# Kernel tuning notes

Hardware: AMD Instinct MI355X
Metric: run time of the kernel (lower is better)

The kernel has to match this reference:

```python
import jax, jax.numpy as jnp
import numpy as np

B, S, E = 2, 2048, 1024
H = 16
D = E // H  # 64
SCALE = D ** -0.5


def setup_inputs() -> dict:
    key = jax.random.key(0)
    ks = jax.random.split(key, 9)
    w = lambda k: jax.random.normal(k, (E, E), dtype=jnp.float32) * 0.02
    b = lambda k: jax.random.normal(k, (E,), dtype=jnp.float32) * 0.02
    return {
        "hidden_states": jax.random.normal(ks[0], (B, S, E), dtype=jnp.float32),
        "q_w": w(ks[1]), "q_b": b(ks[2]),
        "k_w": w(ks[3]), "k_b": b(ks[4]),
        "v_w": w(ks[5]), "v_b": b(ks[6]),
        "o_w": w(ks[7]), "o_b": b(ks[8]),
    }


def reference(hidden_states, q_w, q_b, k_w, k_b, v_w, v_b, o_w, o_b):
    dtype = hidden_states.dtype
    # torch Linear: y = x @ W^T + b
    q = hidden_states @ q_w.T + q_b
    k = hidden_states @ k_w.T + k_b
    v = hidden_states @ v_w.T + v_b
    # [B,S,E] -> [B*H, S, D]
    split = lambda t: t.reshape(B, S, H, D).transpose(0, 2, 1, 3).reshape(B * H, S, D)
    q, k, v = split(q), split(k), split(v)
    # upcast_attention: fp32 QK^T, scaled (baddbmm with beta=0, no mask)
    scores = SCALE * jnp.einsum("bqd,bkd->bqk", q.astype(jnp.float32), k.astype(jnp.float32))
    # upcast_softmax: fp32 softmax over last dim (transpose_qk=False), cast back
    probs = jax.nn.softmax(scores, axis=-1).astype(dtype)
    # PV bmm, merge heads, out_proj (dropout p=0.0 -> identity)
    out = jnp.einsum("bqk,bkd->bqd", probs, v)
    out = out.reshape(B, H, S, D).transpose(0, 2, 1, 3).reshape(B, S, E)
    return out @ o_w.T + o_b
```

## Files before the change

kernel.cpp:

```cpp
#include <hip/hip_runtime.h>

typedef __bf16 bf16x8 __attribute__((ext_vector_type(8)));
typedef __bf16 bf16x4 __attribute__((ext_vector_type(4)));
typedef float  f32x4  __attribute__((ext_vector_type(4)));
typedef float  f32x16 __attribute__((ext_vector_type(16)));
typedef unsigned int u32x4 __attribute__((ext_vector_type(4)));

#define CS 0.18033688011112042f

__device__ __forceinline__ float fast_exp2(float x) {
    return __builtin_amdgcn_exp2f(x);
}

__device__ __forceinline__ void gload_lds16(const __bf16* g, __bf16* l) {
    __builtin_amdgcn_global_load_lds(
        (const __attribute__((address_space(1))) void*)g,
        (__attribute__((address_space(3))) void*)l, 16, 0, 0);
}

__device__ __forceinline__ f32x4 MFMA(bf16x8 a, bf16x8 b, f32x4 c) {
    return __builtin_amdgcn_mfma_f32_16x16x32_bf16(a, b, c, 0, 0, 0);
}
__device__ __forceinline__ f32x16 MFMA32(bf16x8 a, bf16x8 b, f32x16 c) {
    return __builtin_amdgcn_mfma_f32_32x32x16_bf16(a, b, c, 0, 0, 0);
}

__device__ __forceinline__ unsigned pk2(float a, float b) {
    union { __bf16 h[2]; unsigned u; } x;
    x.h[0] = (__bf16)a; x.h[1] = (__bf16)b;
    return x.u;
}

__device__ __forceinline__ void swap32(unsigned &a, unsigned &b) {
    asm volatile("v_permlane32_swap_b32 %0, %1" : "+v"(a), "+v"(b));
}

__global__ __launch_bounds__(256) void cvt5_kernel(
    const float* __restrict__ s0, const float* __restrict__ s1,
    const float* __restrict__ s2, const float* __restrict__ s3,
    const float* __restrict__ s4,
    __bf16* __restrict__ d0, __bf16* __restrict__ d1, __bf16* __restrict__ d2,
    __bf16* __restrict__ d3, __bf16* __restrict__ d4)
{
    int blk = blockIdx.x;
    const float* src; __bf16* dst; int base;
    if (blk < 4096)      { src = s0; dst = d0; base = blk; }
    else if (blk < 5120) { src = s1; dst = d1; base = blk - 4096; }
    else if (blk < 6144) { src = s2; dst = d2; base = blk - 5120; }
    else if (blk < 7168) { src = s3; dst = d3; base = blk - 6144; }
    else                 { src = s4; dst = d4; base = blk - 7168; }
    int i = base * 1024 + threadIdx.x * 4;
    float4 v = *(const float4*)(src + i);
    bf16x4 o;
    o[0] = (__bf16)v.x; o[1] = (__bf16)v.y; o[2] = (__bf16)v.z; o[3] = (__bf16)v.w;
    *(bf16x4*)(dst + i) = o;
}

template <typename OutT, int BN>
__device__ __forceinline__ void gemm_core(const __bf16* __restrict__ A,
                                          const __bf16* __restrict__ W,
                                          const float* __restrict__ bias,
                                          OutT* __restrict__ C,
                                          int m0, int n0, bool vtrans, float oscale)
{
    constexpr int NJ  = BN / 32;
    constexpr int BCH = BN / 32;
    __shared__ __bf16 As[128 * 64];
    __shared__ __bf16 Bs[BN * 64];

    const int tid  = threadIdx.x;
    const int lane = tid & 63;
    const int w    = tid >> 6;
    const int wm   = w & 1;
    const int wn   = w >> 1;
    const int s    = lane & 15;
    const int q    = lane >> 4;

    const int srow = lane >> 3;
    const int scol = (lane & 7) ^ srow;

    f32x4 acc[4][NJ];
#pragma unroll
    for (int i = 0; i < 4; i++)
#pragma unroll
        for (int j = 0; j < NJ; j++)
#pragma unroll
            for (int r = 0; r < 4; r++) acc[i][j][r] = 0.0f;

    for (int k0 = 0; k0 < 1024; k0 += 64) {
        __syncthreads();
#pragma unroll
        for (int t = 0; t < 4; t++) {
            int chunk = w * 4 + t;
            int row   = chunk * 8 + srow;
            gload_lds16(A + (size_t)(m0 + row) * 1024 + k0 + scol * 8,
                        &As[chunk * 512]);
        }
#pragma unroll
        for (int t = 0; t < BCH; t++) {
            int chunk = w * BCH + t;
            int row   = chunk * 8 + srow;
            gload_lds16(W + (size_t)(n0 + row) * 1024 + k0 + scol * 8,
                        &Bs[chunk * 512]);
        }
        __syncthreads();

#pragma unroll
        for (int kk = 0; kk < 2; kk++) {
            bf16x8 af[4], bf[NJ];
#pragma unroll
            for (int i = 0; i < 4; i++) {
                int row = wm * 64 + i * 16 + s;
                af[i] = *(const bf16x8*)&As[row * 64 + ((((kk << 2) + q) ^ (row & 7)) << 3)];
            }
#pragma unroll
            for (int j = 0; j < NJ; j++) {
                int row = wn * (BN / 2) + j * 16 + s;
                bf[j] = *(const bf16x8*)&Bs[row * 64 + ((((kk << 2) + q) ^ (row & 7)) << 3)];
            }
#pragma unroll
            for (int i = 0; i < 4; i++)
#pragma unroll
                for (int j = 0; j < NJ; j++)
                    acc[i][j] = MFMA(af[i], bf[j], acc[i][j]);
        }
    }

    if (vtrans) {
        __bf16* Vt = (__bf16*)C;
#pragma unroll
        for (int j = 0; j < NJ; j++) {
            int col = n0 + wn * (BN / 2) + j * 16 + s;
            int h   = col >> 6;
            int d   = col & 63;
            float bv = bias[col];
#pragma unroll
            for (int i = 0; i < 4; i++) {
                int rowb = m0 + wm * 64 + i * 16 + q * 4;
                int b    = rowb >> 11;
                int sr   = rowb & 2047;
                bf16x4 pk;
#pragma unroll
                for (int r = 0; r < 4; r++) pk[r] = (__bf16)(acc[i][j][r] + bv);
                *(bf16x4*)&Vt[(size_t)((b * 16 + h) * 64 + d) * 2048 + sr] = pk;
            }
        }
    } else {
#pragma unroll
        for (int j = 0; j < NJ; j++) {
            int col = n0 + wn * (BN / 2) + j * 16 + s;
            float bv = bias[col];
#pragma unroll
            for (int i = 0; i < 4; i++) {
                int rowb = m0 + wm * 64 + i * 16 + q * 4;
#pragma unroll
                for (int r = 0; r < 4; r++) {
                    C[(size_t)(rowb + r) * 1024 + col] = (OutT)((acc[i][j][r] + bv) * oscale);
                }
            }
        }
    }
}

__global__ __launch_bounds__(256) void gemm_qkv_kernel(
    const __bf16* __restrict__ X,
    const __bf16* __restrict__ Wq, const float* __restrict__ bq,
    const __bf16* __restrict__ Wk, const float* __restrict__ bk,
    const __bf16* __restrict__ Wv, const float* __restrict__ bv,
    __bf16* __restrict__ Q, __bf16* __restrict__ K, __bf16* __restrict__ Vt)
{
    int mt   = blockIdx.x & 31;
    int ntot = blockIdx.x >> 5;
    int which = ntot >> 3;
    const __bf16* W    = (which == 0) ? Wq : (which == 1) ? Wk : Wv;
    const float*  bias = (which == 0) ? bq : (which == 1) ? bk : bv;
    __bf16*       Out  = (which == 0) ? Q  : (which == 1) ? K  : Vt;
    float oscale = (which == 0) ? CS : 1.0f;
    gemm_core<__bf16, 128>(X, W, bias, Out, mt * 128, (ntot & 7) * 128, which == 2, oscale);
}

__global__ __launch_bounds__(256) void gemm_o_kernel(
    const __bf16* __restrict__ Ain, const __bf16* __restrict__ Wo,
    const float* __restrict__ bo, float* __restrict__ Out)
{
    int mt = blockIdx.x & 31;
    int nt = blockIdx.x >> 5;
    gemm_core<float, 64>(Ain, Wo, bo, Out, mt * 128, nt * 64, false, 1.0f);
}

__global__ __launch_bounds__(512, 4) void attn_kernel(
    const __bf16* __restrict__ Q, const __bf16* __restrict__ K,
    const __bf16* __restrict__ Vt, __bf16* __restrict__ O)
{
    __shared__ __bf16 smem[2][2][2][64 * 64];

    const int bh = blockIdx.x >> 4;
    const int qt = blockIdx.x & 15;
    const int b  = bh >> 4;
    const int h  = bh & 15;

    const int tid  = threadIdx.x;
    const int lane = tid & 63;
    const int w    = tid >> 6;
    const int g    = w >> 2;
    const int ws   = w & 3;
    const int lt   = tid & 255;
    const int qc   = lane & 31;
    const int hi   = lane >> 5;

    bf16x8 bq[4];
    {
        const int qrow = qt * 128 + ws * 32 + qc;
        const __bf16* qp = Q + (size_t)(b * 2048 + qrow) * 1024 + h * 64 + hi * 8;
#pragma unroll
        for (int kd = 0; kd < 4; kd++)
            bq[kd] = *(const bf16x8*)(qp + kd * 16);
    }

    const f32x16 fzero = 0.0f;
    f32x16 acc[2];
#pragma unroll
    for (int nb = 0; nb < 2; nb++) acc[nb] = fzero;
    float lst = 0.0f;

    const __bf16* Kbase = K  + (size_t)(b * 2048 + g * 1024) * 1024 + h * 64;
    const __bf16* Vbase = Vt + (size_t)bh * 64 * 2048 + g * 1024;

    bf16x8 kpre[2], vpre[2];
#pragma unroll
    for (int t = 0; t < 2; t++) {
        int c = lt + 256 * t;
        int krow = c >> 3, s16 = c & 7;
        kpre[t] = *(const bf16x8*)(Kbase + (size_t)krow * 1024 + s16 * 8);
        vpre[t] = *(const bf16x8*)(Vbase + (size_t)krow * 2048 + s16 * 8);
    }
#pragma unroll
    for (int t = 0; t < 2; t++) {
        int c = lt + 256 * t;
        int krow = c >> 3, s16 = c & 7;
        *(bf16x8*)&smem[g][0][0][krow * 64 + ((s16 ^ (krow & 7)) << 3)] = kpre[t];
        *(bf16x8*)&smem[g][0][1][krow * 64 + ((s16 ^ (krow & 7)) << 3)] = vpre[t];
    }
#pragma unroll
    for (int t = 0; t < 2; t++) {
        int c = lt + 256 * t;
        int krow = c >> 3, s16 = c & 7;
        kpre[t] = *(const bf16x8*)(Kbase + (size_t)(64 + krow) * 1024 + s16 * 8);
        vpre[t] = *(const bf16x8*)(Vbase + (size_t)krow * 2048 + 64 + s16 * 8);
    }
    __syncthreads();

    int cur = 0;
    for (int kc = 0; kc < 16; kc++) {
        {
            __bf16* kwb = smem[g][cur ^ 1][0];
            __bf16* vwb = smem[g][cur ^ 1][1];
#pragma unroll
            for (int t = 0; t < 2; t++) {
                int c = lt + 256 * t;
                int krow = c >> 3, s16 = c & 7;
                *(bf16x8*)&kwb[krow * 64 + ((s16 ^ (krow & 7)) << 3)] = kpre[t];
                *(bf16x8*)&vwb[krow * 64 + ((s16 ^ (krow & 7)) << 3)] = vpre[t];
            }
        }
        {
            int kb2 = ((kc + 2) & 15) * 64;
#pragma unroll
            for (int t = 0; t < 2; t++) {
                int c = lt + 256 * t;
                int krow = c >> 3, s16 = c & 7;
                kpre[t] = *(const bf16x8*)(Kbase + (size_t)(kb2 + krow) * 1024 + s16 * 8);
                vpre[t] = *(const bf16x8*)(Vbase + (size_t)krow * 2048 + kb2 + s16 * 8);
            }
        }

        const __bf16* kbuf = smem[g][cur][0];
        const __bf16* vbuf = smem[g][cur][1];

        f32x16 sc[2];
#pragma unroll
        for (int mb = 0; mb < 2; mb++) {
            int row = mb * 32 + qc;
            int rsw = row & 7;
            bf16x8 af0 = *(const bf16x8*)&kbuf[row * 64 + ((hi ^ rsw) << 3)];
            __builtin_amdgcn_s_setprio(1);
            sc[mb] = MFMA32(af0, bq[0], fzero);
            __builtin_amdgcn_s_setprio(0);
#pragma unroll
            for (int kd = 1; kd < 4; kd++) {
                bf16x8 af = *(const bf16x8*)&kbuf[row * 64 + ((((kd << 1) | hi) ^ rsw) << 3)];
                __builtin_amdgcn_s_setprio(1);
                sc[mb] = MFMA32(af, bq[kd], sc[mb]);
                __builtin_amdgcn_s_setprio(0);
            }
        }

#pragma unroll
        for (int mb = 0; mb < 2; mb++) {
            float e[16];
#pragma unroll
            for (int r = 0; r < 16; r++)
                e[r] = fast_exp2(sc[mb][r]);
            float s0 = 0.f, s1 = 0.f, s2 = 0.f, s3 = 0.f;
#pragma unroll
            for (int r = 0; r < 16; r += 4) {
                s0 += e[r]; s1 += e[r + 1]; s2 += e[r + 2]; s3 += e[r + 3];
            }
            lst += (s0 + s1) + (s2 + s3);
#pragma unroll
            for (int bb = 0; bb < 2; bb++) {
                unsigned w0 = pk2(e[8 * bb + 0], e[8 * bb + 1]);
                unsigned w1 = pk2(e[8 * bb + 2], e[8 * bb + 3]);
                unsigned w2 = pk2(e[8 * bb + 4], e[8 * bb + 5]);
                unsigned w3 = pk2(e[8 * bb + 6], e[8 * bb + 7]);
                swap32(w0, w2);
                swap32(w1, w3);
                u32x4 pw; pw[0] = w0; pw[1] = w1; pw[2] = w2; pw[3] = w3;
                bf16x8 pa = __builtin_bit_cast(bf16x8, pw);
                int kslot = ((mb << 1) | bb) << 1;
                bf16x8 bv0 = *(const bf16x8*)&vbuf[(0 * 32 + qc) * 64 + (((kslot | hi) ^ (qc & 7)) << 3)];
                bf16x8 bv1 = *(const bf16x8*)&vbuf[(1 * 32 + qc) * 64 + (((kslot | hi) ^ ((32 + qc) & 7)) << 3)];
                __builtin_amdgcn_s_setprio(1);
                acc[0] = MFMA32(pa, bv0, acc[0]);
                acc[1] = MFMA32(pa, bv1, acc[1]);
                __builtin_amdgcn_s_setprio(0);
            }
        }
        __syncthreads();
        cur ^= 1;
    }

    float* cbuf = (float*)&smem[0][0][0][0];
    if (g == 1) {
        float* p = cbuf + ((size_t)ws * 64 + lane) * 36;
        *(f32x16*)(p)      = acc[0];
        *(f32x16*)(p + 16) = acc[1];
        p[32] = lst;
    }
    __syncthreads();
    if (g == 0) {
        float* p = cbuf + ((size_t)ws * 64 + lane) * 36;
        acc[0] += *(const f32x16*)(p);
        acc[1] += *(const f32x16*)(p + 16);
        lst += p[32];

        float lt2 = lst + __shfl_xor(lst, 32);

        const size_t obase = (size_t)(b * 2048 + qt * 128 + ws * 32) * 1024 + h * 64;
#pragma unroll
        for (int r = 0; r < 16; r++) {
            int row_rel = (r & 3) + 8 * (r >> 2) + 4 * hi;
            float lr = __shfl(lt2, row_rel);
            float inv = 1.0f / lr;
#pragma unroll
            for (int nb = 0; nb < 2; nb++) {
                O[obase + (size_t)row_rel * 1024 + nb * 32 + qc] = (__bf16)(acc[nb][r] * inv);
            }
        }
    }
}

extern "C" void kernel_launch(void* const* d_in, const int* in_sizes, int n_in,
                              void* d_out, int out_size, void* d_ws, size_t ws_size,
                              hipStream_t stream)
{
    const float* hs = (const float*)d_in[0];
    const float* qw = (const float*)d_in[1];
    const float* qb = (const float*)d_in[2];
    const float* kw = (const float*)d_in[3];
    const float* kb = (const float*)d_in[4];
    const float* vw = (const float*)d_in[5];
    const float* vb = (const float*)d_in[6];
    const float* ow = (const float*)d_in[7];
    const float* ob = (const float*)d_in[8];
    float* out = (float*)d_out;

    char* ws = (char*)d_ws;
    const size_t MB = (size_t)1024 * 1024;
    __bf16* Xb  = (__bf16*)(ws);
    __bf16* Wqb = (__bf16*)(ws +  8 * MB);
    __bf16* Wkb = (__bf16*)(ws + 10 * MB);
    __bf16* Wvb = (__bf16*)(ws + 12 * MB);
    __bf16* Wob = (__bf16*)(ws + 14 * MB);
    __bf16* Qb  = (__bf16*)(ws + 16 * MB);
    __bf16* Kb  = (__bf16*)(ws + 24 * MB);
    __bf16* Vtb = (__bf16*)(ws + 32 * MB);
    __bf16* Ab  = (__bf16*)(ws + 40 * MB);

    cvt5_kernel<<<dim3(8192), dim3(256), 0, stream>>>(hs, qw, kw, vw, ow,
                                                      Xb, Wqb, Wkb, Wvb, Wob);

    gemm_qkv_kernel<<<dim3(768), dim3(256), 0, stream>>>(Xb, Wqb, qb, Wkb, kb, Wvb, vb,
                                                         Qb, Kb, Vtb);
    attn_kernel<<<dim3(512), dim3(512), 0, stream>>>(Qb, Kb, Vtb, Ab);
    gemm_o_kernel<<<dim3(512), dim3(256), 0, stream>>>(Ab, Wob, ob, out);
}
```

Measured before the change: 197.6 us.

## Stage K/V tiles with direct global-to-LDS loads instead of register prefetch

Replaces the register-staged double-buffer prefetch of K and V tiles, which used global loads into registers followed by swizzled LDS stores, with buffer_load-to-LDS (global_load_lds) writes of the next tile. The XOR swizzle is moved onto the global address side so that each wave's contiguous LDS writes land in the swizzled layout. This removes the register pressure of the prefetch arrays and the explicit LDS store instructions. The prefetch distance drops from two tiles to one, so there is less latency hiding, and the code relies on the barrier placement to make the async LDS writes visible in time.

```diff
diff --git a/kernel.cpp b/kernel.cpp
--- a/kernel.cpp
+++ b/kernel.cpp
@@ -204,9 +204,12 @@
     const int w    = tid >> 6;
     const int g    = w >> 2;
     const int ws   = w & 3;
-    const int lt   = tid & 255;
+    const int gv   = w & 3;
     const int qc   = lane & 31;
     const int hi   = lane >> 5;
+
+    const int lr8 = lane >> 3;
+    const int pcb = lane & 7;
 
     bf16x8 bq[4];
     {
@@ -226,53 +229,27 @@
     const __bf16* Kbase = K  + (size_t)(b * 2048 + g * 1024) * 1024 + h * 64;
     const __bf16* Vbase = Vt + (size_t)bh * 64 * 2048 + g * 1024;
 
-    bf16x8 kpre[2], vpre[2];
-#pragma unroll
-    for (int t = 0; t < 2; t++) {
-        int c = lt + 256 * t;
-        int krow = c >> 3, s16 = c & 7;
-        kpre[t] = *(const bf16x8*)(Kbase + (size_t)krow * 1024 + s16 * 8);
-        vpre[t] = *(const bf16x8*)(Vbase + (size_t)krow * 2048 + s16 * 8);
-    }
-#pragma unroll
-    for (int t = 0; t < 2; t++) {
-        int c = lt + 256 * t;
-        int krow = c >> 3, s16 = c & 7;
-        *(bf16x8*)&smem[g][0][0][krow * 64 + ((s16 ^ (krow & 7)) << 3)] = kpre[t];
-        *(bf16x8*)&smem[g][0][1][krow * 64 + ((s16 ^ (krow & 7)) << 3)] = vpre[t];
-    }
-#pragma unroll
-    for (int t = 0; t < 2; t++) {
-        int c = lt + 256 * t;
-        int krow = c >> 3, s16 = c & 7;
-        kpre[t] = *(const bf16x8*)(Kbase + (size_t)(64 + krow) * 1024 + s16 * 8);
-        vpre[t] = *(const bf16x8*)(Vbase + (size_t)krow * 2048 + 64 + s16 * 8);
-    }
+    auto stage = [&](int bf, int kb) {
+        __bf16* kdst = smem[g][bf][0];
+        __bf16* vdst = smem[g][bf][1];
+#pragma unroll
+        for (int t = 0; t < 2; t++) {
+            int sc  = gv * 2 + t;
+            int r   = sc * 8 + lr8;
+            int lcb = pcb ^ (r & 7);
+            gload_lds16(Kbase + (size_t)(kb + r) * 1024 + lcb * 8,
+                        kdst + sc * 512);
+            gload_lds16(Vbase + (size_t)r * 2048 + kb + lcb * 8,
+                        vdst + sc * 512);
+        }
+    };
+
+    stage(0, 0);
     __syncthreads();
 
     int cur = 0;
     for (int kc = 0; kc < 16; kc++) {
-        {
-            __bf16* kwb = smem[g][cur ^ 1][0];
-            __bf16* vwb = smem[g][cur ^ 1][1];
-#pragma unroll
-            for (int t = 0; t < 2; t++) {
-                int c = lt + 256 * t;
-                int krow = c >> 3, s16 = c & 7;
-                *(bf16x8*)&kwb[krow * 64 + ((s16 ^ (krow & 7)) << 3)] = kpre[t];
-                *(bf16x8*)&vwb[krow * 64 + ((s16 ^ (krow & 7)) << 3)] = vpre[t];
-            }
-        }
-        {
-            int kb2 = ((kc + 2) & 15) * 64;
-#pragma unroll
-            for (int t = 0; t < 2; t++) {
-                int c = lt + 256 * t;
-                int krow = c >> 3, s16 = c & 7;
-                kpre[t] = *(const bf16x8*)(Kbase + (size_t)(kb2 + krow) * 1024 + s16 * 8);
-                vpre[t] = *(const bf16x8*)(Vbase + (size_t)krow * 2048 + kb2 + s16 * 8);
-            }
-        }
+        stage(cur ^ 1, ((kc + 1) & 15) * 64);
 
         const __bf16* kbuf = smem[g][cur][0];
         const __bf16* vbuf = smem[g][cur][1];
```

Result: no change. 195.2 us (-1.2%).
